# Kernel tuning notes

Hardware: AMD Instinct MI355X
Metric: run time of the kernel (lower is better)

Reference implementation:

```python
import jax, jax.numpy as jnp
import numpy as np

H = 768        # bert hidden_size
HID = 512      # lstm_hidden
HALF = HID // 2
T = 20         # tagset_size
START, STOP = 18, 19
S = 16386      # input positions incl. CLS/SEP
NEG = -10000.0


def setup_inputs() -> dict:
    key = jax.random.key(0)
    ks = jax.random.split(key, 12)
    sc_x = 1.0
    x = jax.random.normal(ks[0], (1, S, H), dtype=jnp.float32)
    # PyTorch LSTM params (gate order i,f,g,o), one layer, bidirectional
    s_ih = 1.0 / np.sqrt(HALF)
    w_ih_f = jax.random.uniform(ks[1], (4 * HALF, H), jnp.float32, -s_ih, s_ih)
    w_hh_f = jax.random.uniform(ks[2], (4 * HALF, HALF), jnp.float32, -s_ih, s_ih)
    b_ih_f = jax.random.uniform(ks[3], (4 * HALF,), jnp.float32, -s_ih, s_ih)
    b_hh_f = jax.random.uniform(ks[4], (4 * HALF,), jnp.float32, -s_ih, s_ih)
    w_ih_b = jax.random.uniform(ks[5], (4 * HALF, H), jnp.float32, -s_ih, s_ih)
    w_hh_b = jax.random.uniform(ks[6], (4 * HALF, HALF), jnp.float32, -s_ih, s_ih)
    b_ih_b = jax.random.uniform(ks[7], (4 * HALF,), jnp.float32, -s_ih, s_ih)
    b_hh_b = jax.random.uniform(ks[8], (4 * HALF,), jnp.float32, -s_ih, s_ih)
    s_t = 1.0 / np.sqrt(HID)
    w_tag = jax.random.uniform(ks[9], (T, HID), jnp.float32, -s_t, s_t)
    b_tag = jax.random.uniform(ks[10], (T,), jnp.float32, -s_t, s_t)
    transitions = jax.random.normal(ks[11], (T, T), dtype=jnp.float32)
    transitions = transitions.at[START, :].set(NEG).at[:, STOP].set(NEG)
    return {
        "x": x,
        "w_ih_f": w_ih_f, "w_hh_f": w_hh_f, "b_ih_f": b_ih_f, "b_hh_f": b_hh_f,
        "w_ih_b": w_ih_b, "w_hh_b": w_hh_b, "b_ih_b": b_ih_b, "b_hh_b": b_hh_b,
        "w_tag": w_tag, "b_tag": b_tag, "transitions": transitions,
    }


def _lstm_one_step(xt, w_ih, b_ih, b_hh):
    # Original passes [1, N, H] to a batch_first=False LSTM => seq_len=1,
    # batch=N, zero initial state. So each token does ONE cell step:
    # h0=c0=0 => hh contribution is only b_hh.
    g = xt @ w_ih.T + b_ih + b_hh          # [N, 4*HALF]
    i, f, gg, o = jnp.split(g, 4, axis=-1)  # PyTorch gate order i,f,g,o
    c = jax.nn.sigmoid(i) * jnp.tanh(gg)    # f*c0 = 0
    return jax.nn.sigmoid(o) * jnp.tanh(c)  # [N, HALF]


def reference(x, w_ih_f, w_hh_f, b_ih_f, b_hh_f,
              w_ih_b, w_hh_b, b_ih_b, b_hh_b,
              w_tag, b_tag, transitions):
    tok = x[0, 1:-1, :]                     # narrow(1,1,S-2): drop CLS/SEP -> [N,H]
    h_f = _lstm_one_step(tok, w_ih_f, b_ih_f, b_hh_f)
    h_b = _lstm_one_step(tok, w_ih_b, b_ih_b, b_hh_b)
    enc = jnp.concatenate([h_f, h_b], axis=-1)   # [N, HID]
    feats = enc @ w_tag.T + b_tag                # [N, T] emission scores

    # ---- Viterbi decode (sequential DP over tokens) ----
    init = jnp.full((T,), NEG, dtype=feats.dtype).at[START].set(0.0)

    def vstep(fv, feat):
        scores = fv[None, :] + transitions       # [next_tag, prev_tag]
        bp = jnp.argmax(scores, axis=1)          # backpointers [T]
        fv_new = jnp.max(scores, axis=1) + feat
        return fv_new, bp

    fv, bps = jax.lax.scan(vstep, init, feats)   # bps: [N, T]
    terminal = fv + transitions[STOP]
    best = jnp.argmax(terminal)
    path_score = terminal[best]

    def btrack(b, bp):
        return bp[b], b                          # emit tag at time t, move to t-1

    _, best_path = jax.lax.scan(btrack, best, bps, reverse=True)  # [N] in time order
    return path_score, best_path
```

## Files before the change

kernel.cpp:

```cpp
#include <hip/hip_runtime.h>
#include <math.h>

#define HDIM 768
#define HIDD 512
#define NTOK 16384
#define NT 20
#define CHUNKS 128
#define CLEN 128

typedef unsigned short ushort_t;
typedef __attribute__((ext_vector_type(8))) short bf16x8;
typedef __attribute__((ext_vector_type(4))) float f32x4;

__device__ __forceinline__ float sigm(float x){ return 1.0f/(1.0f+expf(-x)); }

__device__ __forceinline__ ushort_t f2bf(float f){
    unsigned int u = __float_as_uint(f);
    unsigned int r = (u + 0x7fffu + ((u >> 16) & 1u)) >> 16;
    return (ushort_t)r;
}
__device__ __forceinline__ float bf2f(ushort_t b){
    return __uint_as_float(((unsigned int)b) << 16);
}

#define GLD16(gp, lp) __builtin_amdgcn_global_load_lds( \
    (const __attribute__((address_space(1))) void*)(gp), \
    (__attribute__((address_space(3))) void*)(lp), 16, 0, 0)

__global__ __launch_bounds__(256) void conv_kernel(
    const float* __restrict__ x,
    const float* __restrict__ wf, const float* __restrict__ wb,
    ushort_t* __restrict__ Ah, ushort_t* __restrict__ Al,
    ushort_t* __restrict__ Bh, ushort_t* __restrict__ Bl)
{
    const int bid = blockIdx.x;
    if (bid < 1152){
        int t = bid*256 + threadIdx.x;
        int n = t / 192, c4 = (t - n*192)*4;
        int dir = n / 768, nr = n - dir*768;
        int gate = nr >> 8, j = nr & 255;
        int wrow = j + ((gate==0)?0:((gate==1)?512:768));
        const float* src = dir ? wb : wf;
        const float4 v = *(const float4*)(src + (size_t)wrow*HDIM + c4);
        float f[4] = {v.x, v.y, v.z, v.w};
        ushort_t h[4], l[4];
        #pragma unroll
        for (int i=0;i<4;++i){
            h[i] = f2bf(f[i]);
            l[i] = f2bf(f[i] - bf2f(h[i]));
        }
        *(ushort4*)(Bh + (size_t)n*HDIM + c4) = make_ushort4(h[0],h[1],h[2],h[3]);
        *(ushort4*)(Bl + (size_t)n*HDIM + c4) = make_ushort4(l[0],l[1],l[2],l[3]);
    } else {
        int t = (bid-1152)*256 + threadIdx.x;
        int row = t / 192, c4 = (t - row*192)*4;
        const float4 v = *(const float4*)(x + (size_t)(row+1)*HDIM + c4);
        float f[4] = {v.x, v.y, v.z, v.w};
        ushort_t h[4], l[4];
        #pragma unroll
        for (int i=0;i<4;++i){
            h[i] = f2bf(f[i]);
            l[i] = f2bf(f[i] - bf2f(h[i]));
        }
        *(ushort4*)(Ah + (size_t)row*HDIM + c4) = make_ushort4(h[0],h[1],h[2],h[3]);
        *(ushort4*)(Al + (size_t)row*HDIM + c4) = make_ushort4(l[0],l[1],l[2],l[3]);
    }
}

__global__ __launch_bounds__(256, 2) void gemm_fused(
    const ushort_t* __restrict__ Ah, const ushort_t* __restrict__ Al,
    const ushort_t* __restrict__ Bh, const ushort_t* __restrict__ Bl,
    const float* __restrict__ bihf, const float* __restrict__ bhhf,
    const float* __restrict__ bihb, const float* __restrict__ bhhb,
    const float* __restrict__ wtag, float* __restrict__ featsp)
{
    __shared__ __align__(16) char smem[65536];
    float* hbuf = (float*)smem;
    float* wts  = (float*)(smem + 8448);

    const int tid = threadIdx.x;
    const int bx = blockIdx.x;
    const int xcd = bx & 7, bidx = bx >> 3;
    const int q = bidx & 7, mt = (bidx >> 3)*8 + xcd;
    const int dir = q >> 2, j0 = (q & 3)*64;
    const int row0 = mt*64;
    const float* __restrict__ bih = dir ? bihb : bihf;
    const float* __restrict__ bhh = dir ? bhhb : bhhf;

    const int lane = tid & 63, wv = tid >> 6;
    const int wm = wv >> 1, wn = wv & 1;
    const int lm = lane & 15, lq = lane >> 4;
    const int wbB = (tid & 192) * 16;

    const int P_ = tid >> 3, s_ = tid & 7;
    const int q_ = s_ ^ (P_ & 7);
    const int mA = (P_ << 1) | (q_ >> 2);
    const int k8s = q_ & 3;
    const size_t aoff = (size_t)(row0 + mA)*HDIM + k8s*8;
    size_t bOff[3];
    #pragma unroll
    for (int g=0; g<3; ++g)
        bOff[g] = (size_t)(dir*768 + g*256 + j0 + mA)*HDIM + k8s*8;

    int aoffB[2], boffB[2];
    #pragma unroll
    for (int f=0; f<2; ++f){
        int m = wm*32 + f*16 + lm;
        aoffB[f] = ((m>>1)*8 + ((((m&1)<<2)|lq) ^ ((m>>1)&7)))*16;
        int n = wn*32 + f*16 + lm;
        boffB[f] = ((n>>1)*8 + ((((n&1)<<2)|lq) ^ ((n>>1)&7)))*16;
    }

    int jcol[2];
    #pragma unroll
    for (int f=0; f<2; ++f) jcol[f] = j0 + wn*32 + f*16 + lm;

    f32x4 acc[3][2][2];
    #pragma unroll
    for (int g=0; g<3; ++g)
        #pragma unroll
        for (int fm=0; fm<2; ++fm)
            #pragma unroll
            for (int fn=0; fn<2; ++fn)
                acc[g][fm][fn] = (f32x4){0.f,0.f,0.f,0.f};

    {
        GLD16(Ah + aoff, smem + wbB);
        GLD16(Al + aoff, smem + 4096 + wbB);
        char* bb = smem + 16384;
        #pragma unroll
        for (int g=0; g<3; ++g){
            GLD16(Bh + bOff[g], bb + g*8192 + wbB);
            GLD16(Bl + bOff[g], bb + g*8192 + 4096 + wbB);
        }
    }

    #pragma unroll 1
    for (int kt=0; kt<24; ++kt){
        __syncthreads();

        if (kt < 23){
            const int k0n = (kt+1)*32;
            char* ab = smem + ((kt+1)&1)*8192;
            char* bb = smem + 16384 + ((kt+1)&1)*24576;
            GLD16(Ah + aoff + k0n, ab + wbB);
            GLD16(Al + aoff + k0n, ab + 4096 + wbB);
            #pragma unroll
            for (int g=0; g<3; ++g){
                GLD16(Bh + bOff[g] + k0n, bb + g*8192 + wbB);
                GLD16(Bl + bOff[g] + k0n, bb + g*8192 + 4096 + wbB);
            }
        }

        const char* ab = smem + (kt&1)*8192;
        const char* bb = smem + 16384 + (kt&1)*24576;
        bf16x8 afh[2], afl[2];
        #pragma unroll
        for (int f=0; f<2; ++f){
            afh[f] = *(const bf16x8*)(ab + aoffB[f]);
            afl[f] = *(const bf16x8*)(ab + 4096 + aoffB[f]);
        }
        #pragma unroll
        for (int g=0; g<3; ++g){
            const char* bg = bb + g*8192;
            #pragma unroll
            for (int fn=0; fn<2; ++fn){
                bf16x8 bh = *(const bf16x8*)(bg + boffB[fn]);
                bf16x8 bl = *(const bf16x8*)(bg + 4096 + boffB[fn]);
                #pragma unroll
                for (int fm=0; fm<2; ++fm){
                    acc[g][fm][fn] = __builtin_amdgcn_mfma_f32_16x16x32_bf16(
                        afh[fm], bh, acc[g][fm][fn], 0, 0, 0);
                    acc[g][fm][fn] = __builtin_amdgcn_mfma_f32_16x16x32_bf16(
                        afl[fm], bh, acc[g][fm][fn], 0, 0, 0);
                    acc[g][fm][fn] = __builtin_amdgcn_mfma_f32_16x16x32_bf16(
                        afh[fm], bl, acc[g][fm][fn], 0, 0, 0);
                }
            }
        }
    }

    float bi[2], bg_[2], bo[2];
    #pragma unroll
    for (int f=0; f<2; ++f){
        bi[f]  = bih[jcol[f]]       + bhh[jcol[f]];
        bg_[f] = bih[512 + jcol[f]] + bhh[512 + jcol[f]];
        bo[f]  = bih[768 + jcol[f]] + bhh[768 + jcol[f]];
    }
    float hv[2][2][4];
    #pragma unroll
    for (int fm=0; fm<2; ++fm)
        #pragma unroll
        for (int fn=0; fn<2; ++fn)
            #pragma unroll
            for (int r=0; r<4; ++r){
                float cv = sigm(acc[0][fm][fn][r] + bi[fn]) *
                           tanhf(acc[1][fm][fn][r] + bg_[fn]);
                hv[fm][fn][r] = sigm(acc[2][fm][fn][r] + bo[fn]) * tanhf(cv);
            }

    __syncthreads();
    for (int i2=tid; i2<NT*64; i2+=256){
        int t = i2 >> 6, j = i2 & 63;
        wts[i2] = wtag[t*HIDD + dir*256 + j0 + j];
    }
    float* fq = featsp + (size_t)q * (NTOK*NT);
    #pragma unroll 1
    for (int ph=0; ph<2; ++ph){
        __syncthreads();
        if (wm == ph){
            #pragma unroll
            for (int fm=0; fm<2; ++fm)
                #pragma unroll
                for (int fn=0; fn<2; ++fn)
                    #pragma unroll
                    for (int r=0; r<4; ++r){
                        int mloc = fm*16 + lq*4 + r;
                        int jloc = wn*32 + fn*16 + lm;
                        hbuf[mloc*65 + jloc] = hv[fm][fn][r];
                    }
        }
        __syncthreads();
        const int mrow = tid & 31, grp = tid >> 5;
        if (grp < 5){
            const int tg0 = grp*4;
            float s[4] = {0.f,0.f,0.f,0.f};
            for (int j=0;j<64;++j){
                float h = hbuf[mrow*65 + j];
                #pragma unroll
                for (int tt=0; tt<4; ++tt)
                    s[tt] = fmaf(h, wts[(tg0+tt)*64 + j], s[tt]);
            }
            const int mglob = row0 + ph*32 + mrow;
            #pragma unroll
            for (int tt=0; tt<4; ++tt)
                fq[(size_t)mglob*NT + tg0 + tt] = s[tt];
        }
    }
}

__device__ __forceinline__ void load_fl(
    const float* __restrict__ featsp, const float* __restrict__ btg,
    float* fl, int c, int tid, int nthr)
{
    const int base = c*(CLEN*NT/4);
    for (int idx=tid; idx<CLEN*NT/4; idx+=nthr){
        float4 s[8];
        #pragma unroll
        for (int p=0; p<8; ++p)
            s[p] = ((const float4*)(featsp + (size_t)p*NTOK*NT))[base+idx];
        float4 v;
        v.x = ((s[0].x+s[1].x)+(s[2].x+s[3].x)) + ((s[4].x+s[5].x)+(s[6].x+s[7].x));
        v.y = ((s[0].y+s[1].y)+(s[2].y+s[3].y)) + ((s[4].y+s[5].y)+(s[6].y+s[7].y));
        v.z = ((s[0].z+s[1].z)+(s[2].z+s[3].z)) + ((s[4].z+s[5].z)+(s[6].z+s[7].z));
        v.w = ((s[0].w+s[1].w)+(s[2].w+s[3].w)) + ((s[4].w+s[5].w)+(s[6].w+s[7].w));
        int t0 = (idx*4) % 20;
        v.x += btg[t0]; v.y += btg[t0+1]; v.z += btg[t0+2]; v.w += btg[t0+3];
        ((float4*)fl)[idx] = v;
    }
}

__global__ __launch_bounds__(512) void vit_chunkmat(
    const float* __restrict__ featsp, const float* __restrict__ btag,
    const float* __restrict__ trans, float* __restrict__ Pall)
{
    __shared__ float fl[CLEN*NT];
    __shared__ float Pb[2][NT*NT];
    const int c = blockIdx.x, tid = threadIdx.x;
    load_fl(featsp, btag, fl, c, tid, 512);
    const bool act = tid < NT*NT;
    const int i = tid/20, j = tid - i*20;
    float tr[NT];
    if (act){
        #pragma unroll
        for (int k=0;k<NT;++k) tr[k] = trans[i*NT+k];
        Pb[0][tid] = (i==j) ? 0.f : -1e30f;
    }
    __syncthreads();
    int cur = 0;
    for (int t=0;t<CLEN;++t){
        float m = -3.0e38f;
        if (act){
            #pragma unroll
            for (int k=0;k<NT;++k) m = fmaxf(m, tr[k] + Pb[cur][k*NT+j]);
            m += fl[t*NT+i];
            Pb[cur^1][tid] = m;
        }
        __syncthreads();
        cur ^= 1;
    }
    if (act) Pall[(size_t)c*(NT*NT) + tid] = Pb[cur][tid];
}

__global__ __launch_bounds__(128) void vit_replay(
    const float* __restrict__ featsp, const float* __restrict__ btag,
    const float* __restrict__ trans, const float* __restrict__ Pall,
    unsigned int* __restrict__ bpout, int* __restrict__ Hout,
    float* __restrict__ dout, int* __restrict__ bestws)
{
    __shared__ float fl[CLEN*NT];
    __shared__ float fv[NT];
    __shared__ float Pb[NT*NT];
    __shared__ unsigned char bp[CLEN*NT];
    const int c = blockIdx.x, tid = threadIdx.x;
    load_fl(featsp, btag, fl, c, tid, 128);
    if (tid<NT) fv[tid] = (tid==18) ? 0.f : -10000.f;
    float4 pn = {0.f,0.f,0.f,0.f};
    if (tid<100 && c>0) pn = ((const float4*)Pall)[tid];
    __syncthreads();
    for (int cc=0; cc<c; ++cc){
        if (tid<100) ((float4*)Pb)[tid] = pn;
        if (tid<100 && cc+1<c) pn = ((const float4*)(Pall + (size_t)(cc+1)*(NT*NT)))[tid];
        __syncthreads();
        float nf = -3.0e38f;
        if (tid<NT){
            #pragma unroll
            for (int j=0;j<NT;++j) nf = fmaxf(nf, Pb[tid*NT+j] + fv[j]);
        }
        __syncthreads();
        if (tid<NT) fv[tid] = nf;
        __syncthreads();
    }
    float tr[NT];
    if (tid<NT){
        #pragma unroll
        for (int k=0;k<NT;++k) tr[k] = trans[tid*NT+k];
    }
    __syncthreads();
    for (int t=0;t<CLEN;++t){
        float best = 0.f; int bj = 0;
        if (tid<NT){
            best = tr[0] + fv[0];
            #pragma unroll
            for (int j=1;j<NT;++j){
                float v = tr[j] + fv[j];
                if (v > best){ best = v; bj = j; }
            }
        }
        __syncthreads();
        if (tid<NT){
            fv[tid] = best + fl[t*NT+tid];
            bp[t*NT+tid] = (unsigned char)bj;
        }
        __syncthreads();
    }
    for (int idx=tid; idx<CLEN*NT/4; idx+=128)
        bpout[(size_t)c*(CLEN*NT/4) + idx] = ((unsigned int*)bp)[idx];
    if (tid<NT){
        int m = tid;
        for (int t=CLEN-1;t>=0;--t) m = bp[t*NT+m];
        Hout[c*NT+tid] = m;
    }
    if (c == CHUNKS-1 && tid == 0){
        float best = -3.0e38f; int bidx = 0;
        for (int j=0;j<NT;++j){
            float tv = fv[j] + trans[19*NT+j];
            if (tv > best){ best = tv; bidx = j; }
        }
        dout[0] = best;
        bestws[0] = bidx;
    }
}

__global__ __launch_bounds__(64) void bt_fill(
    const unsigned int* __restrict__ bpin, const int* __restrict__ Hin,
    const int* __restrict__ bestws, float* __restrict__ dout)
{
    __shared__ int Hl[CHUNKS*NT];
    __shared__ unsigned char bp[CLEN*NT];
    __shared__ float ob[CLEN];
    const int c = blockIdx.x, tid = threadIdx.x;
    for (int idx=tid; idx<CHUNKS*NT; idx+=64) Hl[idx] = Hin[idx];
    for (int idx=tid; idx<CLEN*NT/4; idx+=64)
        ((unsigned int*)bp)[idx] = bpin[(size_t)c*(CLEN*NT/4) + idx];
    __syncthreads();
    if (tid==0){
        int e = bestws[0];
        for (int cc=CHUNKS-1; cc>c; --cc) e = Hl[cc*NT+e];
        for (int t=CLEN-1;t>=0;--t){ ob[t] = (float)e; e = bp[t*NT+e]; }
    }
    __syncthreads();
    for (int idx=tid; idx<CLEN; idx+=64)
        dout[1 + c*CLEN + idx] = ob[idx];
}

extern "C" void kernel_launch(void* const* d_in, const int* in_sizes, int n_in,
                              void* d_out, int out_size, void* d_ws, size_t ws_size,
                              hipStream_t stream)
{
    const float* x    = (const float*)d_in[0];
    const float* wf   = (const float*)d_in[1];
    const float* bihf = (const float*)d_in[3];
    const float* bhhf = (const float*)d_in[4];
    const float* wb   = (const float*)d_in[5];
    const float* bihb = (const float*)d_in[7];
    const float* bhhb = (const float*)d_in[8];
    const float* wtag = (const float*)d_in[9];
    const float* btag = (const float*)d_in[10];
    const float* trans= (const float*)d_in[11];
    float* out = (float*)d_out;

    char* w = (char*)d_ws;
    ushort_t* Ah = (ushort_t*)w;         w += 25165824;
    ushort_t* Al = (ushort_t*)w;         w += 25165824;
    ushort_t* Bh = (ushort_t*)w;         w += 2359296;
    ushort_t* Bl = (ushort_t*)w;         w += 2359296;
    float* featsp = (float*)w;           w += 10485760;
    float* Pall  = (float*)w;            w += 204800;
    int* Hmap    = (int*)w;              w += 10240;
    unsigned int* bp = (unsigned int*)w; w += 327680;
    int* best    = (int*)w;

    conv_kernel<<<13440, 256, 0, stream>>>(x, wf, wb, Ah, Al, Bh, Bl);
    gemm_fused<<<2048, 256, 0, stream>>>(Ah, Al, Bh, Bl, bihf, bhhf, bihb, bhhb,
                                         wtag, featsp);
    vit_chunkmat<<<CHUNKS, 512, 0, stream>>>(featsp, btag, trans, Pall);
    vit_replay<<<CHUNKS, 128, 0, stream>>>(featsp, btag, trans, Pall, bp, Hmap,
                                           out, best);
    bt_fill<<<CHUNKS, 64, 0, stream>>>(bp, Hmap, best, out);
}
```

Before: 391.7 us.

## Double GEMM M-tile to 128 rows and hoist chunk-prefix Viterbi scan

The fused LSTM GEMM now computes 128 rows per block instead of 64, with four M fragments per wave and 80KB of shared memory. This halves the grid and reuses each loaded B tile for twice as many rows. Separately, the O(c) prefix max-plus scan that every vit_replay block repeated is moved into a single vit_scan kernel, which writes each chunk's starting forward vector once. The costs are more registers and LDS per block, likely lower occupancy, and one extra serial kernel launch.

```diff
diff --git a/kernel.cpp b/kernel.cpp
--- a/kernel.cpp
+++ b/kernel.cpp
@@ -74,16 +74,16 @@
     const float* __restrict__ bihb, const float* __restrict__ bhhb,
     const float* __restrict__ wtag, float* __restrict__ featsp)
 {
-    __shared__ __align__(16) char smem[65536];
+    __shared__ __align__(16) char smem[81920];
     float* hbuf = (float*)smem;
-    float* wts  = (float*)(smem + 8448);
+    float* wts  = (float*)(smem + 16640);
 
     const int tid = threadIdx.x;
     const int bx = blockIdx.x;
-    const int xcd = bx & 7, bidx = bx >> 3;
-    const int q = bidx & 7, mt = (bidx >> 3)*8 + xcd;
+    const int xcd = bx & 7, g3 = bx >> 3;
+    const int q = g3 & 7, mt = (g3 >> 3)*8 + xcd;
     const int dir = q >> 2, j0 = (q & 3)*64;
-    const int row0 = mt*64;
+    const int row0 = mt*128;
     const float* __restrict__ bih = dir ? bihb : bihf;
     const float* __restrict__ bhh = dir ? bhhb : bhhf;
 
@@ -96,17 +96,22 @@
     const int q_ = s_ ^ (P_ & 7);
     const int mA = (P_ << 1) | (q_ >> 2);
     const int k8s = q_ & 3;
-    const size_t aoff = (size_t)(row0 + mA)*HDIM + k8s*8;
+    const size_t aoff0 = (size_t)(row0 + mA)*HDIM + k8s*8;
+    const size_t aoff1 = (size_t)(row0 + 64 + mA)*HDIM + k8s*8;
     size_t bOff[3];
     #pragma unroll
     for (int g=0; g<3; ++g)
         bOff[g] = (size_t)(dir*768 + g*256 + j0 + mA)*HDIM + k8s*8;
 
-    int aoffB[2], boffB[2];
+    int aoffB[4], boffB[2];
+    #pragma unroll
+    for (int f=0; f<4; ++f){
+        int m = wm*64 + f*16 + lm;
+        int rg = m >> 6, r = m & 63;
+        aoffB[f] = rg*4096 + ((r>>1)*8 + ((((r&1)<<2)|lq) ^ ((r>>1)&7)))*16;
+    }
     #pragma unroll
     for (int f=0; f<2; ++f){
-        int m = wm*32 + f*16 + lm;
-        aoffB[f] = ((m>>1)*8 + ((((m&1)<<2)|lq) ^ ((m>>1)&7)))*16;
         int n = wn*32 + f*16 + lm;
         boffB[f] = ((n>>1)*8 + ((((n&1)<<2)|lq) ^ ((n>>1)&7)))*16;
     }
@@ -115,19 +120,21 @@
     #pragma unroll
     for (int f=0; f<2; ++f) jcol[f] = j0 + wn*32 + f*16 + lm;
 
-    f32x4 acc[3][2][2];
+    f32x4 acc[3][4][2];
     #pragma unroll
     for (int g=0; g<3; ++g)
         #pragma unroll
-        for (int fm=0; fm<2; ++fm)
+        for (int fm=0; fm<4; ++fm)
             #pragma unroll
             for (int fn=0; fn<2; ++fn)
                 acc[g][fm][fn] = (f32x4){0.f,0.f,0.f,0.f};
 
     {
-        GLD16(Ah + aoff, smem + wbB);
-        GLD16(Al + aoff, smem + 4096 + wbB);
-        char* bb = smem + 16384;
+        GLD16(Ah + aoff0, smem + wbB);
+        GLD16(Ah + aoff1, smem + 4096 + wbB);
+        GLD16(Al + aoff0, smem + 8192 + wbB);
+        GLD16(Al + aoff1, smem + 12288 + wbB);
+        char* bb = smem + 32768;
         #pragma unroll
         for (int g=0; g<3; ++g){
             GLD16(Bh + bOff[g], bb + g*8192 + wbB);
@@ -141,10 +148,12 @@
 
         if (kt < 23){
             const int k0n = (kt+1)*32;
-            char* ab = smem + ((kt+1)&1)*8192;
-            char* bb = smem + 16384 + ((kt+1)&1)*24576;
-            GLD16(Ah + aoff + k0n, ab + wbB);
-            GLD16(Al + aoff + k0n, ab + 4096 + wbB);
+            char* ab = smem + ((kt+1)&1)*16384;
+            char* bb = smem + 32768 + ((kt+1)&1)*24576;
+            GLD16(Ah + aoff0 + k0n, ab + wbB);
+            GLD16(Ah + aoff1 + k0n, ab + 4096 + wbB);
+            GLD16(Al + aoff0 + k0n, ab + 8192 + wbB);
+            GLD16(Al + aoff1 + k0n, ab + 12288 + wbB);
             #pragma unroll
             for (int g=0; g<3; ++g){
                 GLD16(Bh + bOff[g] + k0n, bb + g*8192 + wbB);
@@ -152,13 +161,13 @@
             }
         }
 
-        const char* ab = smem + (kt&1)*8192;
-        const char* bb = smem + 16384 + (kt&1)*24576;
-        bf16x8 afh[2], afl[2];
-        #pragma unroll
-        for (int f=0; f<2; ++f){
+        const char* ab = smem + (kt&1)*16384;
+        const char* bb = smem + 32768 + (kt&1)*24576;
+        bf16x8 afh[4], afl[4];
+        #pragma unroll
+        for (int f=0; f<4; ++f){
             afh[f] = *(const bf16x8*)(ab + aoffB[f]);
-            afl[f] = *(const bf16x8*)(ab + 4096 + aoffB[f]);
+            afl[f] = *(const bf16x8*)(ab + 8192 + aoffB[f]);
         }
         #pragma unroll
         for (int g=0; g<3; ++g){
@@ -168,7 +177,7 @@
                 bf16x8 bh = *(const bf16x8*)(bg + boffB[fn]);
                 bf16x8 bl = *(const bf16x8*)(bg + 4096 + boffB[fn]);
                 #pragma unroll
-                for (int fm=0; fm<2; ++fm){
+                for (int fm=0; fm<4; ++fm){
                     acc[g][fm][fn] = __builtin_amdgcn_mfma_f32_16x16x32_bf16(
                         afh[fm], bh, acc[g][fm][fn], 0, 0, 0);
                     acc[g][fm][fn] = __builtin_amdgcn_mfma_f32_16x16x32_bf16(
@@ -187,9 +196,9 @@
         bg_[f] = bih[512 + jcol[f]] + bhh[512 + jcol[f]];
         bo[f]  = bih[768 + jcol[f]] + bhh[768 + jcol[f]];
     }
-    float hv[2][2][4];
-    #pragma unroll
-    for (int fm=0; fm<2; ++fm)
+    float hv[4][2][4];
+    #pragma unroll
+    for (int fm=0; fm<4; ++fm)
         #pragma unroll
         for (int fn=0; fn<2; ++fn)
             #pragma unroll
@@ -210,7 +219,7 @@
         __syncthreads();
         if (wm == ph){
             #pragma unroll
-            for (int fm=0; fm<2; ++fm)
+            for (int fm=0; fm<4; ++fm)
                 #pragma unroll
                 for (int fn=0; fn<2; ++fn)
                     #pragma unroll
@@ -221,21 +230,19 @@
                     }
         }
         __syncthreads();
-        const int mrow = tid & 31, grp = tid >> 5;
-        if (grp < 5){
-            const int tg0 = grp*4;
-            float s[4] = {0.f,0.f,0.f,0.f};
-            for (int j=0;j<64;++j){
-                float h = hbuf[mrow*65 + j];
-                #pragma unroll
-                for (int tt=0; tt<4; ++tt)
-                    s[tt] = fmaf(h, wts[(tg0+tt)*64 + j], s[tt]);
-            }
-            const int mglob = row0 + ph*32 + mrow;
-            #pragma unroll
-            for (int tt=0; tt<4; ++tt)
-                fq[(size_t)mglob*NT + tg0 + tt] = s[tt];
-        }
+        const int mrow = tid & 63, grp = tid >> 6;
+        const int tg0 = grp*5;
+        float s[5] = {0.f,0.f,0.f,0.f,0.f};
+        for (int j=0;j<64;++j){
+            float h = hbuf[mrow*65 + j];
+            #pragma unroll
+            for (int tt=0; tt<5; ++tt)
+                s[tt] = fmaf(h, wts[(tg0+tt)*64 + j], s[tt]);
+        }
+        const int mglob = row0 + ph*64 + mrow;
+        #pragma unroll
+        for (int tt=0; tt<5; ++tt)
+            fq[(size_t)mglob*NT + tg0 + tt] = s[tt];
     }
 }
 
@@ -292,37 +299,54 @@
     if (act) Pall[(size_t)c*(NT*NT) + tid] = Pb[cur][tid];
 }
 
+__global__ __launch_bounds__(128) void vit_scan(
+    const float* __restrict__ Pall, const float* __restrict__ trans,
+    float* __restrict__ fvstart, float* __restrict__ dout, int* __restrict__ bestws)
+{
+    __shared__ float Pb[NT*NT];
+    __shared__ float fv[NT];
+    const int tid = threadIdx.x;
+    float4 pn = {0.f,0.f,0.f,0.f};
+    if (tid<100) pn = ((const float4*)Pall)[tid];
+    if (tid<NT) fv[tid] = (tid==18) ? 0.f : -10000.f;
+    for (int c=0;c<CHUNKS;++c){
+        if (tid<100) ((float4*)Pb)[tid] = pn;
+        if (tid<100 && c+1<CHUNKS) pn = ((const float4*)(Pall + (size_t)(c+1)*(NT*NT)))[tid];
+        __syncthreads();
+        if (tid<NT) fvstart[c*NT+tid] = fv[tid];
+        float nf = -3.0e38f;
+        if (tid<NT){
+            #pragma unroll
+            for (int j=0;j<NT;++j) nf = fmaxf(nf, Pb[tid*NT+j] + fv[j]);
+        }
+        __syncthreads();
+        if (tid<NT) fv[tid] = nf;
+    }
+    __syncthreads();
+    if (tid==0){
+        float best = -3.0e38f; int bidx = 0;
+        for (int j=0;j<NT;++j){
+            float tv = fv[j] + trans[19*NT+j];
+            if (tv > best){ best = tv; bidx = j; }
+        }
+        dout[0] = best;
+        bestws[0] = bidx;
+    }
+}
+
 __global__ __launch_bounds__(128) void vit_replay(
     const float* __restrict__ featsp, const float* __restrict__ btag,
-    const float* __restrict__ trans, const float* __restrict__ Pall,
-    unsigned int* __restrict__ bpout, int* __restrict__ Hout,
-    float* __restrict__ dout, int* __restrict__ bestws)
+    const float* __restrict__ trans, const float* __restrict__ fvstart,
+    unsigned int* __restrict__ bpout, int* __restrict__ Hout)
 {
     __shared__ float fl[CLEN*NT];
     __shared__ float fv[NT];
-    __shared__ float Pb[NT*NT];
     __shared__ unsigned char bp[CLEN*NT];
     const int c = blockIdx.x, tid = threadIdx.x;
     load_fl(featsp, btag, fl, c, tid, 128);
-    if (tid<NT) fv[tid] = (tid==18) ? 0.f : -10000.f;
-    float4 pn = {0.f,0.f,0.f,0.f};
-    if (tid<100 && c>0) pn = ((const float4*)Pall)[tid];
-    __syncthreads();
-    for (int cc=0; cc<c; ++cc){
-        if (tid<100) ((float4*)Pb)[tid] = pn;
-        if (tid<100 && cc+1<c) pn = ((const float4*)(Pall + (size_t)(cc+1)*(NT*NT)))[tid];
-        __syncthreads();
-        float nf = -3.0e38f;
-        if (tid<NT){
-            #pragma unroll
-            for (int j=0;j<NT;++j) nf = fmaxf(nf, Pb[tid*NT+j] + fv[j]);
-        }
-        __syncthreads();
-        if (tid<NT) fv[tid] = nf;
-        __syncthreads();
-    }
     float tr[NT];
     if (tid<NT){
+        fv[tid] = fvstart[c*NT+tid];
         #pragma unroll
         for (int k=0;k<NT;++k) tr[k] = trans[tid*NT+k];
     }
@@ -350,15 +374,6 @@
         int m = tid;
         for (int t=CLEN-1;t>=0;--t) m = bp[t*NT+m];
         Hout[c*NT+tid] = m;
-    }
-    if (c == CHUNKS-1 && tid == 0){
-        float best = -3.0e38f; int bidx = 0;
-        for (int j=0;j<NT;++j){
-            float tv = fv[j] + trans[19*NT+j];
-            if (tv > best){ best = tv; bidx = j; }
-        }
-        dout[0] = best;
-        bestws[0] = bidx;
     }
 }
 
@@ -407,15 +422,16 @@
     ushort_t* Bl = (ushort_t*)w;         w += 2359296;
     float* featsp = (float*)w;           w += 10485760;
     float* Pall  = (float*)w;            w += 204800;
+    float* fvst  = (float*)w;            w += 10240;
     int* Hmap    = (int*)w;              w += 10240;
     unsigned int* bp = (unsigned int*)w; w += 327680;
     int* best    = (int*)w;
 
     conv_kernel<<<13440, 256, 0, stream>>>(x, wf, wb, Ah, Al, Bh, Bl);
-    gemm_fused<<<2048, 256, 0, stream>>>(Ah, Al, Bh, Bl, bihf, bhhf, bihb, bhhb,
+    gemm_fused<<<1024, 256, 0, stream>>>(Ah, Al, Bh, Bl, bihf, bhhf, bihb, bhhb,
                                          wtag, featsp);
     vit_chunkmat<<<CHUNKS, 512, 0, stream>>>(featsp, btag, trans, Pall);
-    vit_replay<<<CHUNKS, 128, 0, stream>>>(featsp, btag, trans, Pall, bp, Hmap,
-                                           out, best);
+    vit_scan<<<1, 128, 0, stream>>>(Pall, trans, fvst, out, best);
+    vit_replay<<<CHUNKS, 128, 0, stream>>>(featsp, btag, trans, fvst, bp, Hmap);
     bt_fill<<<CHUNKS, 64, 0, stream>>>(bp, Hmap, best, out);
 }
```

Measured after the change: 368.9 us. 1.06x faster.
